# Kernel optimization log

Hardware: AMD Instinct MI355X
Metric: run time of the kernel (lower is better)

Reference implementation:

```python
import jax, jax.numpy as jnp
import numpy as np

B, T, HE, L, HD = 512, 512, 512, 64, 512

def setup_inputs() -> dict:
    key = jax.random.key(0)
    ks = jax.random.split(key, 16)
    def w(k, shape):
        return jax.random.normal(k, shape, dtype=jnp.float32) * 0.05
    z32 = lambda n: jnp.zeros((n,), jnp.float32)
    return {
        "input_tensor": jax.random.normal(ks[0], (B, T, 1), dtype=jnp.float32),
        # encoder LSTMCell (keras gate order i, f, g, o)
        "enc_W": w(ks[1], (1, 4 * HE)),
        "enc_U": w(ks[2], (HE, 4 * HE)),
        "enc_b": z32(4 * HE),
        # encoder mu / std heads
        "emu_W": w(ks[3], (HE, L)), "emu_b": z32(L),
        "estd_W": w(ks[4], (HE, L)), "estd_b": z32(L),
        # decoder first-state dense (tanh)
        "dfs_W": w(ks[5], (L, HD)), "dfs_b": z32(HD),
        # decoder LSTMCell
        "dec_W": w(ks[6], (L, 4 * HD)),
        "dec_U": w(ks[7], (HD, 4 * HD)),
        "dec_b": z32(4 * HD),
        # decoder mu / std heads (Dense(1))
        "dmu_W": w(ks[8], (HD, 1)), "dmu_b": z32(1),
        "dstd_W": w(ks[9], (HD, 1)), "dstd_b": z32(1),
    }

def _lstm_update(gates, c):
    i, f, g, o = jnp.split(gates, 4, axis=-1)
    c_new = jax.nn.sigmoid(f) * c + jax.nn.sigmoid(i) * jnp.tanh(g)
    h_new = jax.nn.sigmoid(o) * jnp.tanh(c_new)
    return h_new, c_new

def reference(input_tensor, enc_W, enc_U, enc_b, emu_W, emu_b, estd_W, estd_b,
              dfs_W, dfs_b, dec_W, dec_U, dec_b, dmu_W, dmu_b, dstd_W, dstd_b):
    x = input_tensor
    Bn, Tn = x.shape[0], x.shape[1]
    He = enc_U.shape[0]

    # ---- encoder: LSTM over time, keep final h ----
    def enc_step(carry, xt):
        h, c = carry
        gates = xt @ enc_W + h @ enc_U + enc_b
        return _lstm_update(gates, c), None
    h0 = jnp.zeros((Bn, He), x.dtype)
    (hT, _), _ = jax.lax.scan(enc_step, (h0, h0), jnp.swapaxes(x, 0, 1))

    mu_enc = hT @ emu_W + emu_b                       # [B, L]
    sigma_enc = jax.nn.softplus(hT @ estd_W + estd_b)  # [B, L]
    z = mu_enc  # call() uses reparam=False -> latent returns mu

    # ---- decoder: LSTM fed constant z each step ----
    hd = jnp.tanh(z @ dfs_W + dfs_b)                  # [B, HD]
    cd = jnp.zeros_like(hd)
    zin = z @ dec_W + dec_b                           # input projection constant over t
    def dec_step(carry, _):
        h, c = carry
        h_new, c_new = _lstm_update(zin + h @ dec_U, c)
        mu = h_new @ dmu_W + dmu_b                    # [B, 1]
        sg = h_new @ dstd_W + dstd_b
        return (h_new, c_new), (mu, sg)
    _, (mus, sgs) = jax.lax.scan(dec_step, (hd, cd), None, length=Tn)

    mu_dec = jnp.swapaxes(mus, 0, 1)                  # [B, T, 1]
    sigma_dec = jax.nn.softplus(jnp.swapaxes(sgs, 0, 1))
    return (mu_dec, sigma_dec, mu_enc, sigma_enc)
```

## Files before the change

### kernel.cpp

```cpp
#include <hip/hip_runtime.h>


#define B_   512
#define T_   512
#define H_   512
#define NGR  32
#define WPG  8
#define RPG  16
#define UPW  64

typedef _Float16 f16;
typedef _Float16 f16x8 __attribute__((ext_vector_type(8)));
typedef _Float16 f16x4 __attribute__((ext_vector_type(4)));
typedef float f32x16 __attribute__((ext_vector_type(16)));
typedef unsigned long long u64;

#define OFF_SG_DEC 262144
#define OFF_MU_ENC 524288
#define OFF_SG_ENC 557056

__device__ __forceinline__ float sigm_(float x) { return 1.f / (1.f + __expf(-x)); }
__device__ __forceinline__ float tanh_(float x) {
  float t = fabsf(x);
  float e = __expf(2.f * t);
  float r = 1.f - 2.f / (e + 1.f);
  return x < 0.f ? -r : r;
}
__device__ __forceinline__ float softplus_(float x) {
  return fmaxf(x, 0.f) + log1pf(__expf(-fabsf(x)));
}

__global__ void pack_U(const float* __restrict__ U, f16* __restrict__ Upk) {
  const int e = blockIdx.x * 256 + threadIdx.x;
  const int j = e & 7, lane = (e >> 3) & 63, ks = (e >> 9) & 31;
  const int w = (e >> 14) & 7, wg = (e >> 17) & 7;
  const int ccol = lane & 31, khalf = lane >> 5;
  const int uu = ccol >> 2, gate = ccol & 3;
  const int k = ks * 16 + khalf * 8 + j;
  const int gcol = gate * 512 + wg * UPW + w * 8 + uu;
  Upk[e] = (f16)U[k * 2048 + gcol];
}

template <int IS_DEC>
__global__ void __launch_bounds__(512, 1)
lstm_rec(const f16* __restrict__ Upk,
         const float* __restrict__ xin,
         const float* __restrict__ wa,
         const float* __restrict__ wb,
         f16* __restrict__ hbuf,
         float* __restrict__ accmu,
         float* __restrict__ accsg,
         int* __restrict__ flags) {
  const int bid = blockIdx.x;
  const int wg = (bid >> 3) & 7;
  const int g = (bid & 7) * 4 + (bid >> 6);
  const int tid = threadIdx.x;
  const int wave = tid >> 6, lane = tid & 63;
  const int R0 = g * RPG;
  const int U0 = wg * UPW;

  const int ccol = lane & 31, khalf = lane >> 5;
  f16x8 Breg[32];
#pragma unroll
  for (int ks = 0; ks < 32; ++ks) {
    const f16* p = Upk + (((wg * 8 + wave) * 32 + ks) << 9) + lane * 8;
    asm volatile("global_load_dwordx4 %0, %1, off\n\ts_waitcnt vmcnt(0)"
                 : "=v"(Breg[ks]) : "v"(p));
  }

  const int row = tid >> 4;
  const int q = (tid & 15) * 4;
  float addv[16], xw[16], dmur[4], dstdr[4];
  if (tid < 256) {
#pragma unroll
    for (int m = 0; m < 4; ++m) {
#pragma unroll
      for (int gt = 0; gt < 4; ++gt) {
        const int col = gt * 512 + U0 + q + m;
        if (IS_DEC) {
          addv[m * 4 + gt] = xin[(R0 + row) * 2048 + col];
          xw[m * 4 + gt] = 0.f;
        } else {
          addv[m * 4 + gt] = wb[col];
          xw[m * 4 + gt] = wa[col];
        }
      }
      if (IS_DEC) {
        dmur[m] = wa[U0 + q + m];
        dstdr[m] = wb[U0 + q + m];
      } else {
        dmur[m] = 0.f;
        dstdr[m] = 0.f;
      }
    }
  }

  float cst[4] = {0.f, 0.f, 0.f, 0.f};

  __shared__ __align__(16) f16 hstage[RPG * 536];
  __shared__ float gatesLds[RPG * 260];
  __shared__ float pmuLds[RPG * 17];
  __shared__ float psgLds[RPG * 17];
  __shared__ float xl[RPG * 516];

  if (!IS_DEC) {
#pragma unroll
    for (int i = 0; i < 16; ++i) {
      const int idx = tid + i * 512;
      const int r = idx >> 9, c2 = idx & 511;
      xl[r * 516 + c2] = xin[(R0 + r) * T_ + c2];
    }
    __syncthreads();
  }

  const int hrow = lane & 15;
  int* const myflag = &flags[(g * WPG + wg) * 32];
  int* const grpflags = &flags[(g * WPG) * 32];

  for (int t = 0; t < T_; ++t) {
    const u64* hsrc64 = (const u64*)(hbuf + (t & 1) * (B_ * H_) + R0 * H_);
#pragma unroll
    for (int i = 0; i < 4; ++i) {
      const int w = tid + i * 512;
      const int r = w >> 7, c8 = w & 127;
      u64 v = __hip_atomic_load(hsrc64 + w, __ATOMIC_RELAXED,
                                __HIP_MEMORY_SCOPE_AGENT);
      *(u64*)&hstage[r * 536 + c8 * 4] = v;
    }
    __syncthreads();

    f32x16 acc;
#pragma unroll
    for (int j = 0; j < 16; ++j) acc[j] = 0.f;
#pragma unroll
    for (int ks = 0; ks < 32; ++ks) {
      f16x8 a = *(const f16x8*)&hstage[hrow * 536 + ks * 16 + khalf * 8];
      acc = __builtin_amdgcn_mfma_f32_32x32x16_f16(a, Breg[ks], acc, 0, 0, 0);
    }
#pragma unroll
    for (int r = 0; r < 8; ++r) {
      const int orow = (r & 3) + 8 * (r >> 2) + 4 * khalf;
      gatesLds[orow * 260 + wave * 32 + ccol] = acc[r];
    }
    __syncthreads();

    union { f16x4 h4; u64 u; } cv;
    if (tid < 256) {
      float xv = 0.f;
      if (!IS_DEC) xv = xl[row * 516 + t];
      float hn[4];
#pragma unroll
      for (int m = 0; m < 4; ++m) {
        float ga[4];
#pragma unroll
        for (int gt = 0; gt < 4; ++gt) {
          float v = gatesLds[row * 260 + (q + m) * 4 + gt] + addv[m * 4 + gt];
          if (!IS_DEC) v += xv * xw[m * 4 + gt];
          ga[gt] = v;
        }
        const float iv = sigm_(ga[0]);
        const float fv = sigm_(ga[1]);
        const float gv = tanh_(ga[2]);
        const float ov = sigm_(ga[3]);
        const float cn = fv * cst[m] + iv * gv;
        cst[m] = cn;
        hn[m] = ov * tanh_(cn);
      }
#pragma unroll
      for (int m = 0; m < 4; ++m) cv.h4[m] = (f16)hn[m];
      f16* hdst = hbuf + ((t + 1) & 1) * (B_ * H_) + (R0 + row) * H_ + U0 + q;
      __hip_atomic_store((u64*)hdst, cv.u, __ATOMIC_RELAXED,
                         __HIP_MEMORY_SCOPE_AGENT);
      if (IS_DEC) {
        float pmu = 0.f, psg = 0.f;
#pragma unroll
        for (int m = 0; m < 4; ++m) {
          pmu += (float)cv.h4[m] * dmur[m];
          psg += (float)cv.h4[m] * dstdr[m];
        }
        pmuLds[row * 17 + (tid & 15)] = pmu;
        psgLds[row * 17 + (tid & 15)] = psg;
      }
    }

    asm volatile("s_waitcnt vmcnt(0)" ::: "memory");
    __syncthreads();
    if (t + 1 < T_ && tid == 0)
      __hip_atomic_store(myflag, t + 1, __ATOMIC_RELAXED,
                         __HIP_MEMORY_SCOPE_AGENT);

    if (IS_DEC) {
      if (tid < RPG) {
        float s = 0.f;
#pragma unroll
        for (int j = 0; j < 16; ++j) s += pmuLds[tid * 17 + j];
        unsafeAtomicAdd(&accmu[(R0 + tid) * T_ + t], s);
      } else if (tid < 2 * RPG) {
        const int rr = tid - RPG;
        float s = 0.f;
#pragma unroll
        for (int j = 0; j < 16; ++j) s += psgLds[rr * 17 + j];
        unsafeAtomicAdd(&accsg[(R0 + rr) * T_ + t], s);
      }
    }

    if (t + 1 < T_) {
      if (tid < WPG) {
        while (__hip_atomic_load(&grpflags[tid * 32], __ATOMIC_RELAXED,
                                 __HIP_MEMORY_SCOPE_AGENT) < t + 1) {
          asm volatile("s_sleep 1");
        }
      }
      __syncthreads();
    }
  }
}

__global__ void enc_heads(const f16* __restrict__ h0, const float* __restrict__ emuW,
                          const float* __restrict__ emub, const float* __restrict__ estdW,
                          const float* __restrict__ estdb, float* __restrict__ out,
                          float* __restrict__ z) {
  const int b = blockIdx.x, tid = threadIdx.x;
  __shared__ float hrow[512];
  for (int k = tid; k < 512; k += 128)
    hrow[k] = (float)h0[b * H_ + k];
  __syncthreads();
  const int head = tid >> 6, l = tid & 63;
  const float* W = head ? estdW : emuW;
  float a = 0.f;
#pragma unroll 8
  for (int k = 0; k < 512; ++k) a += hrow[k] * W[k * 64 + l];
  if (head == 0) {
    const float v = a + emub[l];
    out[OFF_MU_ENC + b * 64 + l] = v;
    z[b * 64 + l] = v;
  } else {
    out[OFF_SG_ENC + b * 64 + l] = softplus_(a + estdb[l]);
  }
}

__global__ void dec_prep(const float* __restrict__ z, const float* __restrict__ dfsW,
                         const float* __restrict__ dfsb, const float* __restrict__ decW,
                         const float* __restrict__ decb, f16* __restrict__ hbuf,
                         float* __restrict__ zin) {
  const int b = blockIdx.x, tid = threadIdx.x;
  __shared__ float zl[64];
  if (tid < 64) zl[tid] = z[b * 64 + tid];
  __syncthreads();
  for (int c = tid; c < 512; c += 256) {
    float a = dfsb[c];
#pragma unroll
    for (int l = 0; l < 64; ++l) a += zl[l] * dfsW[l * 512 + c];
    hbuf[b * H_ + c] = (f16)tanh_(a);
  }
  for (int c = tid; c < 2048; c += 256) {
    float a = decb[c];
#pragma unroll
    for (int l = 0; l < 64; ++l) a += zl[l] * decW[l * 2048 + c];
    zin[b * 2048 + c] = a;
  }
}

__global__ void finalize_k(const float* __restrict__ accmu, const float* __restrict__ accsg,
                           const float* __restrict__ dmub, const float* __restrict__ dstdb,
                           float* __restrict__ out) {
  const int i = blockIdx.x * 256 + threadIdx.x;
  out[i] = accmu[i] + dmub[0];
  out[OFF_SG_DEC + i] = softplus_(accsg[i] + dstdb[0]);
}

extern "C" void kernel_launch(void* const* d_in, const int* in_sizes, int n_in,
                              void* d_out, int out_size, void* d_ws, size_t ws_size,
                              hipStream_t stream) {
  (void)in_sizes; (void)n_in; (void)out_size; (void)ws_size;
  const float* x     = (const float*)d_in[0];
  const float* encW  = (const float*)d_in[1];
  const float* encU  = (const float*)d_in[2];
  const float* encb  = (const float*)d_in[3];
  const float* emuW  = (const float*)d_in[4];
  const float* emub  = (const float*)d_in[5];
  const float* estdW = (const float*)d_in[6];
  const float* estdb = (const float*)d_in[7];
  const float* dfsW  = (const float*)d_in[8];
  const float* dfsb  = (const float*)d_in[9];
  const float* decW  = (const float*)d_in[10];
  const float* decb  = (const float*)d_in[12];
  const float* decU  = (const float*)d_in[11];
  const float* dmuW  = (const float*)d_in[13];
  const float* dmub  = (const float*)d_in[14];
  const float* dstdW = (const float*)d_in[15];
  const float* dstdb = (const float*)d_in[16];

  char* ws = (char*)d_ws;
  f16* hbuf    = (f16*)(ws + 0);
  float* accmu = (float*)(ws + (1u << 20));
  float* accsg = (float*)(ws + (2u << 20));
  int* flags   = (int*)(ws + (3u << 20));
  f16* UpkE    = (f16*)(ws + (3u << 20) + 65536);
  float* zin   = (float*)(ws + (3u << 20) + 65536);
  f16* UpkD    = (f16*)(ws + (7u << 20) + 65536);
  float* z     = (float*)(ws + (9u << 20) + 65536);
  float* out   = (float*)d_out;

  hipMemsetAsync(d_ws, 0, (3u << 20) + 65536, stream);

  hipLaunchKernelGGL(pack_U, dim3(4096), dim3(256), 0, stream, encU, UpkE);
  hipLaunchKernelGGL(pack_U, dim3(4096), dim3(256), 0, stream, decU, UpkD);

  hipLaunchKernelGGL((lstm_rec<0>), dim3(256), dim3(512), 0, stream,
                     UpkE, x, encW, encb, hbuf, (float*)nullptr, (float*)nullptr,
                     flags);
  hipLaunchKernelGGL(enc_heads, dim3(512), dim3(128), 0, stream,
                     hbuf, emuW, emub, estdW, estdb, out, z);
  hipLaunchKernelGGL(dec_prep, dim3(512), dim3(256), 0, stream,
                     z, dfsW, dfsb, decW, decb, hbuf, zin);
  hipLaunchKernelGGL((lstm_rec<1>), dim3(256), dim3(512), 0, stream,
                     UpkD, zin, dmuW, dstdW, hbuf, accmu, accsg, flags + 8192);
  hipLaunchKernelGGL(finalize_k, dim3(1024), dim3(256), 0, stream,
                     accmu, accsg, dmub, dstdb, out);
}
```

Before: 4.233 ms.

## Replace per-step flag barrier with generation-tagged h values polled directly

Each fp16 hidden value is now stored in a 32-bit word with a 16-bit generation tag, so consumers spin on the h data itself until every word carries the current step's tag. This removes the separate flag store, the vmcnt drain, and the flag-polling barrier. The next step's loads are issued early, hstage is double-buffered, and the decoder output heads are computed one step late from staged h with wave shuffles instead of atomics, plus a tail kernel for the last step. The cost is twice the bytes per h exchange and busy polling without sleeps.

```diff
diff --git a/kernel.cpp b/kernel.cpp
--- a/kernel.cpp
+++ b/kernel.cpp
@@ -11,9 +11,9 @@
 
 typedef _Float16 f16;
 typedef _Float16 f16x8 __attribute__((ext_vector_type(8)));
-typedef _Float16 f16x4 __attribute__((ext_vector_type(4)));
 typedef float f32x16 __attribute__((ext_vector_type(16)));
 typedef unsigned long long u64;
+typedef unsigned int u32;
 
 #define OFF_SG_DEC 262144
 #define OFF_MU_ENC 524288
@@ -28,6 +28,12 @@
 }
 __device__ __forceinline__ float softplus_(float x) {
   return fmaxf(x, 0.f) + log1pf(__expf(-fabsf(x)));
+}
+__device__ __forceinline__ int fresh_(u64 w, u32 g) {
+  return ((u32)(w >> 48) == g) & (((u32)(w >> 16) & 0xffffu) == g);
+}
+__device__ __forceinline__ u32 packh_(u64 w) {
+  return (u32)(w & 0xffffu) | (((u32)(w >> 32) & 0xffffu) << 16);
 }
 
 __global__ void pack_U(const float* __restrict__ U, f16* __restrict__ Upk) {
@@ -47,10 +53,9 @@
          const float* __restrict__ xin,
          const float* __restrict__ wa,
          const float* __restrict__ wb,
-         f16* __restrict__ hbuf,
+         u32* __restrict__ hbuf,
          float* __restrict__ accmu,
-         float* __restrict__ accsg,
-         int* __restrict__ flags) {
+         float* __restrict__ accsg) {
   const int bid = blockIdx.x;
   const int wg = (bid >> 3) & 7;
   const int g = (bid & 7) * 4 + (bid >> 6);
@@ -58,6 +63,7 @@
   const int wave = tid >> 6, lane = tid & 63;
   const int R0 = g * RPG;
   const int U0 = wg * UPW;
+  const u32 GB = IS_DEC ? 0x8000u : 0u;
 
   const int ccol = lane & 31, khalf = lane >> 5;
   f16x8 Breg[32];
@@ -70,7 +76,7 @@
 
   const int row = tid >> 4;
   const int q = (tid & 15) * 4;
-  float addv[16], xw[16], dmur[4], dstdr[4];
+  float addv[16], xw[16];
   if (tid < 256) {
 #pragma unroll
     for (int m = 0; m < 4; ++m) {
@@ -85,22 +91,21 @@
           xw[m * 4 + gt] = wa[col];
         }
       }
-      if (IS_DEC) {
-        dmur[m] = wa[U0 + q + m];
-        dstdr[m] = wb[U0 + q + m];
-      } else {
-        dmur[m] = 0.f;
-        dstdr[m] = 0.f;
-      }
+    }
+  }
+  float wmu[8], wsg[8];
+  if (IS_DEC) {
+#pragma unroll
+    for (int j = 0; j < 8; ++j) {
+      wmu[j] = wa[lane * 8 + j];
+      wsg[j] = wb[lane * 8 + j];
     }
   }
 
   float cst[4] = {0.f, 0.f, 0.f, 0.f};
 
-  __shared__ __align__(16) f16 hstage[RPG * 536];
+  __shared__ __align__(16) f16 hstage[2][RPG * 536];
   __shared__ float gatesLds[RPG * 260];
-  __shared__ float pmuLds[RPG * 17];
-  __shared__ float psgLds[RPG * 17];
   __shared__ float xl[RPG * 516];
 
   if (!IS_DEC) {
@@ -113,20 +118,43 @@
     __syncthreads();
   }
 
+  int srow[8], scol[8], gidx[8];
+#pragma unroll
+  for (int i = 0; i < 8; ++i) {
+    const int w = tid + i * 512;
+    srow[i] = w >> 8; scol[i] = w & 255;
+    gidx[i] = (R0 + srow[i]) * 256 + scol[i];
+  }
+  const u64* hb64 = (const u64*)hbuf;
   const int hrow = lane & 15;
-  int* const myflag = &flags[(g * WPG + wg) * 32];
-  int* const grpflags = &flags[(g * WPG) * 32];
+
+  u64 wr[8];
+#pragma unroll
+  for (int i = 0; i < 8; ++i)
+    wr[i] = __hip_atomic_load(hb64 + gidx[i], __ATOMIC_RELAXED,
+                              __HIP_MEMORY_SCOPE_AGENT);
+  asm volatile("" ::: "memory");
 
   for (int t = 0; t < T_; ++t) {
-    const u64* hsrc64 = (const u64*)(hbuf + (t & 1) * (B_ * H_) + R0 * H_);
-#pragma unroll
-    for (int i = 0; i < 4; ++i) {
-      const int w = tid + i * 512;
-      const int r = w >> 7, c8 = w & 127;
-      u64 v = __hip_atomic_load(hsrc64 + w, __ATOMIC_RELAXED,
-                                __HIP_MEMORY_SCOPE_AGENT);
-      *(u64*)&hstage[r * 536 + c8 * 4] = v;
-    }
+    const int b0 = (t & 1) * 131072;
+    const int b1 = ((t + 1) & 1) * 131072;
+    const int c1 = ((t + 1) & 1) * 262144;
+    const u32 gr = GB + (u32)t, gn = gr + 1u;
+
+    for (;;) {
+      int f = 1;
+#pragma unroll
+      for (int i = 0; i < 8; ++i) f &= fresh_(wr[i], gr);
+      if (f) break;
+#pragma unroll
+      for (int i = 0; i < 8; ++i)
+        wr[i] = __hip_atomic_load(hb64 + b0 + gidx[i], __ATOMIC_RELAXED,
+                                  __HIP_MEMORY_SCOPE_AGENT);
+    }
+    f16* const sb = hstage[t & 1];
+#pragma unroll
+    for (int i = 0; i < 8; ++i)
+      *(u32*)&sb[srow[i] * 536 + scol[i] * 2] = packh_(wr[i]);
     __syncthreads();
 
     f32x16 acc;
@@ -134,7 +162,7 @@
     for (int j = 0; j < 16; ++j) acc[j] = 0.f;
 #pragma unroll
     for (int ks = 0; ks < 32; ++ks) {
-      f16x8 a = *(const f16x8*)&hstage[hrow * 536 + ks * 16 + khalf * 8];
+      f16x8 a = *(const f16x8*)&sb[hrow * 536 + ks * 16 + khalf * 8];
       acc = __builtin_amdgcn_mfma_f32_32x32x16_f16(a, Breg[ks], acc, 0, 0, 0);
     }
 #pragma unroll
@@ -144,7 +172,6 @@
     }
     __syncthreads();
 
-    union { f16x4 h4; u64 u; } cv;
     if (tid < 256) {
       float xv = 0.f;
       if (!IS_DEC) xv = xl[row * 516 + t];
@@ -166,64 +193,78 @@
         cst[m] = cn;
         hn[m] = ov * tanh_(cn);
       }
-#pragma unroll
-      for (int m = 0; m < 4; ++m) cv.h4[m] = (f16)hn[m];
-      f16* hdst = hbuf + ((t + 1) & 1) * (B_ * H_) + (R0 + row) * H_ + U0 + q;
-      __hip_atomic_store((u64*)hdst, cv.u, __ATOMIC_RELAXED,
-                         __HIP_MEMORY_SCOPE_AGENT);
-      if (IS_DEC) {
-        float pmu = 0.f, psg = 0.f;
-#pragma unroll
-        for (int m = 0; m < 4; ++m) {
-          pmu += (float)cv.h4[m] * dmur[m];
-          psg += (float)cv.h4[m] * dstdr[m];
-        }
-        pmuLds[row * 17 + (tid & 15)] = pmu;
-        psgLds[row * 17 + (tid & 15)] = psg;
-      }
-    }
-
-    asm volatile("s_waitcnt vmcnt(0)" ::: "memory");
-    __syncthreads();
-    if (t + 1 < T_ && tid == 0)
-      __hip_atomic_store(myflag, t + 1, __ATOMIC_RELAXED,
-                         __HIP_MEMORY_SCOPE_AGENT);
-
-    if (IS_DEC) {
-      if (tid < RPG) {
-        float s = 0.f;
-#pragma unroll
-        for (int j = 0; j < 16; ++j) s += pmuLds[tid * 17 + j];
-        unsafeAtomicAdd(&accmu[(R0 + tid) * T_ + t], s);
-      } else if (tid < 2 * RPG) {
-        const int rr = tid - RPG;
-        float s = 0.f;
-#pragma unroll
-        for (int j = 0; j < 16; ++j) s += psgLds[rr * 17 + j];
-        unsafeAtomicAdd(&accsg[(R0 + rr) * T_ + t], s);
-      }
-    }
-
-    if (t + 1 < T_) {
-      if (tid < WPG) {
-        while (__hip_atomic_load(&grpflags[tid * 32], __ATOMIC_RELAXED,
-                                 __HIP_MEMORY_SCOPE_AGENT) < t + 1) {
-          asm volatile("s_sleep 1");
-        }
-      }
-      __syncthreads();
-    }
-  }
-}
-
-__global__ void enc_heads(const f16* __restrict__ h0, const float* __restrict__ emuW,
+      union { f16 h; unsigned short u; } hc0, hc1, hc2, hc3;
+      hc0.h = (f16)hn[0]; hc1.h = (f16)hn[1];
+      hc2.h = (f16)hn[2]; hc3.h = (f16)hn[3];
+      const u64 tg = (u64)gn << 16;
+      const u64 w0 = (tg | hc0.u) | (((tg | hc1.u)) << 32);
+      const u64 w1 = (tg | hc2.u) | (((tg | hc3.u)) << 32);
+      u64* hdst = (u64*)(hbuf + c1 + (R0 + row) * 512 + U0 + q);
+      __hip_atomic_store(hdst, w0, __ATOMIC_RELAXED, __HIP_MEMORY_SCOPE_AGENT);
+      __hip_atomic_store(hdst + 1, w1, __ATOMIC_RELAXED, __HIP_MEMORY_SCOPE_AGENT);
+    }
+
+#pragma unroll
+    for (int i = 0; i < 8; ++i)
+      wr[i] = __hip_atomic_load(hb64 + b1 + gidx[i], __ATOMIC_RELAXED,
+                                __HIP_MEMORY_SCOPE_AGENT);
+    asm volatile("" ::: "memory");
+
+    if (IS_DEC && t >= 1 && wave < 2) {
+      const int hr = 2 * wg + wave;
+      const f16x8 hv = *(const f16x8*)&sb[hr * 536 + lane * 8];
+      float smu = 0.f, ssg = 0.f;
+#pragma unroll
+      for (int j = 0; j < 8; ++j) {
+        const float hq = (float)hv[j];
+        smu += hq * wmu[j]; ssg += hq * wsg[j];
+      }
+#pragma unroll
+      for (int o = 32; o; o >>= 1) {
+        smu += __shfl_xor(smu, o); ssg += __shfl_xor(ssg, o);
+      }
+      if (lane == 0) {
+        accmu[(R0 + hr) * 512 + (t - 1)] = smu;
+        accsg[(R0 + hr) * 512 + (t - 1)] = ssg;
+      }
+    }
+  }
+}
+
+__global__ void dec_tail(const u32* __restrict__ hbuf, const float* __restrict__ dmuW,
+                         const float* __restrict__ dstdW, float* __restrict__ accmu,
+                         float* __restrict__ accsg) {
+  const int r = blockIdx.x, lane = threadIdx.x;
+  float smu = 0.f, ssg = 0.f;
+#pragma unroll
+  for (int j = 0; j < 8; ++j) {
+    union { unsigned short u; f16 h; } c;
+    c.u = (unsigned short)(hbuf[r * 512 + lane * 8 + j] & 0xffffu);
+    const float hq = (float)c.h;
+    smu += hq * dmuW[lane * 8 + j];
+    ssg += hq * dstdW[lane * 8 + j];
+  }
+#pragma unroll
+  for (int o = 32; o; o >>= 1) {
+    smu += __shfl_xor(smu, o); ssg += __shfl_xor(ssg, o);
+  }
+  if (lane == 0) {
+    accmu[r * 512 + 511] = smu;
+    accsg[r * 512 + 511] = ssg;
+  }
+}
+
+__global__ void enc_heads(const u32* __restrict__ h0, const float* __restrict__ emuW,
                           const float* __restrict__ emub, const float* __restrict__ estdW,
                           const float* __restrict__ estdb, float* __restrict__ out,
                           float* __restrict__ z) {
   const int b = blockIdx.x, tid = threadIdx.x;
   __shared__ float hrow[512];
-  for (int k = tid; k < 512; k += 128)
-    hrow[k] = (float)h0[b * H_ + k];
+  for (int k = tid; k < 512; k += 128) {
+    union { unsigned short u; f16 h; } c;
+    c.u = (unsigned short)(h0[b * 512 + k] & 0xffffu);
+    hrow[k] = (float)c.h;
+  }
   __syncthreads();
   const int head = tid >> 6, l = tid & 63;
   const float* W = head ? estdW : emuW;
@@ -241,7 +282,7 @@
 
 __global__ void dec_prep(const float* __restrict__ z, const float* __restrict__ dfsW,
                          const float* __restrict__ dfsb, const float* __restrict__ decW,
-                         const float* __restrict__ decb, f16* __restrict__ hbuf,
+                         const float* __restrict__ decb, u32* __restrict__ hbuf,
                          float* __restrict__ zin) {
   const int b = blockIdx.x, tid = threadIdx.x;
   __shared__ float zl[64];
@@ -251,7 +292,8 @@
     float a = dfsb[c];
 #pragma unroll
     for (int l = 0; l < 64; ++l) a += zl[l] * dfsW[l * 512 + c];
-    hbuf[b * H_ + c] = (f16)tanh_(a);
+    union { f16 h; unsigned short u; } hc; hc.h = (f16)tanh_(a);
+    hbuf[b * 512 + c] = (0x8000u << 16) | (u32)hc.u;
   }
   for (int c = tid; c < 2048; c += 256) {
     float a = decb[c];
@@ -284,38 +326,38 @@
   const float* dfsW  = (const float*)d_in[8];
   const float* dfsb  = (const float*)d_in[9];
   const float* decW  = (const float*)d_in[10];
+  const float* decU  = (const float*)d_in[11];
   const float* decb  = (const float*)d_in[12];
-  const float* decU  = (const float*)d_in[11];
   const float* dmuW  = (const float*)d_in[13];
   const float* dmub  = (const float*)d_in[14];
   const float* dstdW = (const float*)d_in[15];
   const float* dstdb = (const float*)d_in[16];
 
   char* ws = (char*)d_ws;
-  f16* hbuf    = (f16*)(ws + 0);
-  float* accmu = (float*)(ws + (1u << 20));
-  float* accsg = (float*)(ws + (2u << 20));
-  int* flags   = (int*)(ws + (3u << 20));
-  f16* UpkE    = (f16*)(ws + (3u << 20) + 65536);
-  float* zin   = (float*)(ws + (3u << 20) + 65536);
-  f16* UpkD    = (f16*)(ws + (7u << 20) + 65536);
-  float* z     = (float*)(ws + (9u << 20) + 65536);
+  u32*   hbuf  = (u32*)(ws + 0);
+  float* accmu = (float*)(ws + (2u << 20));
+  float* accsg = (float*)(ws + (3u << 20));
+  f16*   UpkE  = (f16*)(ws + (4u << 20));
+  float* zin   = (float*)(ws + (4u << 20));
+  f16*   UpkD  = (f16*)(ws + (8u << 20));
+  float* z     = (float*)(ws + (10u << 20));
   float* out   = (float*)d_out;
 
-  hipMemsetAsync(d_ws, 0, (3u << 20) + 65536, stream);
+  hipMemsetAsync(d_ws, 0, 2u << 20, stream);
 
   hipLaunchKernelGGL(pack_U, dim3(4096), dim3(256), 0, stream, encU, UpkE);
   hipLaunchKernelGGL(pack_U, dim3(4096), dim3(256), 0, stream, decU, UpkD);
 
   hipLaunchKernelGGL((lstm_rec<0>), dim3(256), dim3(512), 0, stream,
-                     UpkE, x, encW, encb, hbuf, (float*)nullptr, (float*)nullptr,
-                     flags);
+                     UpkE, x, encW, encb, hbuf, (float*)nullptr, (float*)nullptr);
   hipLaunchKernelGGL(enc_heads, dim3(512), dim3(128), 0, stream,
                      hbuf, emuW, emub, estdW, estdb, out, z);
   hipLaunchKernelGGL(dec_prep, dim3(512), dim3(256), 0, stream,
                      z, dfsW, dfsb, decW, decb, hbuf, zin);
   hipLaunchKernelGGL((lstm_rec<1>), dim3(256), dim3(512), 0, stream,
-                     UpkD, zin, dmuW, dstdW, hbuf, accmu, accsg, flags + 8192);
+                     UpkD, zin, dmuW, dstdW, hbuf, accmu, accsg);
+  hipLaunchKernelGGL(dec_tail, dim3(512), dim3(64), 0, stream,
+                     hbuf, dmuW, dstdW, accmu, accsg);
   hipLaunchKernelGGL(finalize_k, dim3(1024), dim3(256), 0, stream,
                      accmu, accsg, dmub, dstdb, out);
 }
```

Result: slower. 4.896 ms (+15.7%).

## Replace encoder flag barrier with generation-tagged h values and two-half pipelining

Applied to the files above, without the earlier changes.

The encoder recurrence becomes its own kernel. Each h value is stored as a 32-bit word carrying the fp16 value plus a step tag, so consumers poll the data words directly for freshness instead of waiting on per-group flags and a separate barrier. Each block splits its 16 rows into two 8-row halves and interleaves them, so loading one half's h overlaps the MFMA and gate work of the other. This removes the flag store/poll round trip and adds overlap, at the cost of doubling the h buffer size, spin-polling on data words, and running MFMAs on half-empty tiles.

```diff
diff --git a/kernel.cpp b/kernel.cpp
--- a/kernel.cpp
+++ b/kernel.cpp
@@ -14,6 +14,7 @@
 typedef _Float16 f16x4 __attribute__((ext_vector_type(4)));
 typedef float f32x16 __attribute__((ext_vector_type(16)));
 typedef unsigned long long u64;
+typedef unsigned int u32;
 
 #define OFF_SG_DEC 262144
 #define OFF_MU_ENC 524288
@@ -28,6 +29,12 @@
 }
 __device__ __forceinline__ float softplus_(float x) {
   return fmaxf(x, 0.f) + log1pf(__expf(-fabsf(x)));
+}
+__device__ __forceinline__ int fresh_(u64 w, u32 g) {
+  return ((u32)(w >> 48) == g) & (((u32)(w >> 16) & 0xffffu) == g);
+}
+__device__ __forceinline__ u32 packh_(u64 w) {
+  return (u32)(w & 0xffffu) | (((u32)(w >> 32) & 0xffffu) << 16);
 }
 
 __global__ void pack_U(const float* __restrict__ U, f16* __restrict__ Upk) {
@@ -41,12 +48,172 @@
   Upk[e] = (f16)U[k * 2048 + gcol];
 }
 
-template <int IS_DEC>
 __global__ void __launch_bounds__(512, 1)
-lstm_rec(const f16* __restrict__ Upk,
+lstm_enc(const f16* __restrict__ Upk,
          const float* __restrict__ xin,
          const float* __restrict__ wa,
          const float* __restrict__ wb,
+         u32* __restrict__ hbuf) {
+  const int bid = blockIdx.x;
+  const int s = bid >> 3;
+  const int j = (bid & 7) * 4 + (s & 3);
+  const int wg = s >> 2;
+  const int tid = threadIdx.x, wave = tid >> 6, lane = tid & 63;
+  const int U0 = wg * 64;
+  const int RA = j * 16, RB = j * 16 + 8;
+  const int ccol = lane & 31, khalf = lane >> 5;
+
+  f16x8 Breg[32];
+#pragma unroll
+  for (int ks = 0; ks < 32; ++ks) {
+    const f16* p = Upk + (((wg * 8 + wave) * 32 + ks) << 9) + lane * 8;
+    asm volatile("global_load_dwordx4 %0, %1, off\n\ts_waitcnt vmcnt(0)"
+                 : "=v"(Breg[ks]) : "v"(p));
+  }
+
+  const int erow = tid >> 6, eu = tid & 63;
+  float xwv[4], bias[4];
+#pragma unroll
+  for (int gt = 0; gt < 4; ++gt) {
+    const int col = gt * 512 + U0 + eu;
+    bias[gt] = wb[col];
+    xwv[gt] = wa[col];
+  }
+
+  float cA = 0.f, cB = 0.f;
+
+  __shared__ __align__(16) f16 bufA[8 * 520];
+  __shared__ __align__(16) f16 bufB[8 * 520];
+  __shared__ __align__(16) float gatesL[8 * 264];
+
+  int lrow[4], lcol[4], gidxA[4], gidxB[4];
+#pragma unroll
+  for (int i = 0; i < 4; ++i) {
+    const int w = tid + i * 512;
+    lrow[i] = w >> 8; lcol[i] = w & 255;
+    gidxA[i] = (RA + lrow[i]) * 256 + lcol[i];
+    gidxB[i] = (RB + lrow[i]) * 256 + lcol[i];
+  }
+  const u64* hb64 = (const u64*)hbuf;
+
+  u64 wAr[4], wBr[4];
+#pragma unroll
+  for (int i = 0; i < 4; ++i)
+    wAr[i] = __hip_atomic_load(hb64 + gidxA[i], __ATOMIC_RELAXED,
+                               __HIP_MEMORY_SCOPE_AGENT);
+  asm volatile("" ::: "memory");
+
+  for (int t = 0; t < T_; ++t) {
+    const int b0 = (t & 1) * 131072;
+    const int b1 = ((t + 1) & 1) * 131072;
+    const int c1 = ((t + 1) & 1) * 262144;
+    const u32 gr = (u32)t, gn = (u32)t + 1u;
+
+    while (!(fresh_(wAr[0], gr) & fresh_(wAr[1], gr) &
+             fresh_(wAr[2], gr) & fresh_(wAr[3], gr))) {
+#pragma unroll
+      for (int i = 0; i < 4; ++i)
+        wAr[i] = __hip_atomic_load(hb64 + b0 + gidxA[i], __ATOMIC_RELAXED,
+                                   __HIP_MEMORY_SCOPE_AGENT);
+    }
+#pragma unroll
+    for (int i = 0; i < 4; ++i)
+      *(u32*)&bufA[lrow[i] * 520 + lcol[i] * 2] = packh_(wAr[i]);
+    __syncthreads();
+
+#pragma unroll
+    for (int i = 0; i < 4; ++i)
+      wBr[i] = __hip_atomic_load(hb64 + b0 + gidxB[i], __ATOMIC_RELAXED,
+                                 __HIP_MEMORY_SCOPE_AGENT);
+    asm volatile("" ::: "memory");
+
+    {
+      f32x16 acc;
+#pragma unroll
+      for (int q = 0; q < 16; ++q) acc[q] = 0.f;
+#pragma unroll
+      for (int ks = 0; ks < 32; ++ks) {
+        f16x8 a = *(const f16x8*)&bufA[(lane & 7) * 520 + ks * 16 + khalf * 8];
+        acc = __builtin_amdgcn_mfma_f32_32x32x16_f16(a, Breg[ks], acc, 0, 0, 0);
+      }
+#pragma unroll
+      for (int r = 0; r < 4; ++r)
+        gatesL[(r + 4 * khalf) * 264 + wave * 32 + ccol] = acc[r];
+    }
+    __syncthreads();
+
+    {
+      const float4 g4 = *(const float4*)&gatesL[erow * 264 + (eu >> 3) * 32 + (eu & 7) * 4];
+      const float xv = xin[(RA + erow) * T_ + t];
+      const float ga0 = g4.x + bias[0] + xv * xwv[0];
+      const float ga1 = g4.y + bias[1] + xv * xwv[1];
+      const float ga2 = g4.z + bias[2] + xv * xwv[2];
+      const float ga3 = g4.w + bias[3] + xv * xwv[3];
+      const float cn = sigm_(ga1) * cA + sigm_(ga0) * tanh_(ga2);
+      cA = cn;
+      const float hn = sigm_(ga3) * tanh_(cn);
+      union { f16 h; unsigned short u; } hc; hc.h = (f16)hn;
+      __hip_atomic_store(hbuf + c1 + (RA + erow) * 512 + U0 + eu,
+                         (gn << 16) | (u32)hc.u, __ATOMIC_RELAXED,
+                         __HIP_MEMORY_SCOPE_AGENT);
+    }
+
+    while (!(fresh_(wBr[0], gr) & fresh_(wBr[1], gr) &
+             fresh_(wBr[2], gr) & fresh_(wBr[3], gr))) {
+#pragma unroll
+      for (int i = 0; i < 4; ++i)
+        wBr[i] = __hip_atomic_load(hb64 + b0 + gidxB[i], __ATOMIC_RELAXED,
+                                   __HIP_MEMORY_SCOPE_AGENT);
+    }
+#pragma unroll
+    for (int i = 0; i < 4; ++i)
+      *(u32*)&bufB[lrow[i] * 520 + lcol[i] * 2] = packh_(wBr[i]);
+    __syncthreads();
+
+#pragma unroll
+    for (int i = 0; i < 4; ++i)
+      wAr[i] = __hip_atomic_load(hb64 + b1 + gidxA[i], __ATOMIC_RELAXED,
+                                 __HIP_MEMORY_SCOPE_AGENT);
+    asm volatile("" ::: "memory");
+
+    {
+      f32x16 acc;
+#pragma unroll
+      for (int q = 0; q < 16; ++q) acc[q] = 0.f;
+#pragma unroll
+      for (int ks = 0; ks < 32; ++ks) {
+        f16x8 a = *(const f16x8*)&bufB[(lane & 7) * 520 + ks * 16 + khalf * 8];
+        acc = __builtin_amdgcn_mfma_f32_32x32x16_f16(a, Breg[ks], acc, 0, 0, 0);
+      }
+#pragma unroll
+      for (int r = 0; r < 4; ++r)
+        gatesL[(r + 4 * khalf) * 264 + wave * 32 + ccol] = acc[r];
+    }
+    __syncthreads();
+
+    {
+      const float4 g4 = *(const float4*)&gatesL[erow * 264 + (eu >> 3) * 32 + (eu & 7) * 4];
+      const float xv = xin[(RB + erow) * T_ + t];
+      const float ga0 = g4.x + bias[0] + xv * xwv[0];
+      const float ga1 = g4.y + bias[1] + xv * xwv[1];
+      const float ga2 = g4.z + bias[2] + xv * xwv[2];
+      const float ga3 = g4.w + bias[3] + xv * xwv[3];
+      const float cn = sigm_(ga1) * cB + sigm_(ga0) * tanh_(ga2);
+      cB = cn;
+      const float hn = sigm_(ga3) * tanh_(cn);
+      union { f16 h; unsigned short u; } hc; hc.h = (f16)hn;
+      __hip_atomic_store(hbuf + c1 + (RB + erow) * 512 + U0 + eu,
+                         (gn << 16) | (u32)hc.u, __ATOMIC_RELAXED,
+                         __HIP_MEMORY_SCOPE_AGENT);
+    }
+  }
+}
+
+__global__ void __launch_bounds__(512, 1)
+lstm_dec(const f16* __restrict__ Upk,
+         const float* __restrict__ zin,
+         const float* __restrict__ wmu_,
+         const float* __restrict__ wsg_,
          f16* __restrict__ hbuf,
          float* __restrict__ accmu,
          float* __restrict__ accsg,
@@ -70,28 +237,15 @@
 
   const int row = tid >> 4;
   const int q = (tid & 15) * 4;
-  float addv[16], xw[16], dmur[4], dstdr[4];
+  float addv[16], dmur[4], dstdr[4];
   if (tid < 256) {
 #pragma unroll
     for (int m = 0; m < 4; ++m) {
 #pragma unroll
-      for (int gt = 0; gt < 4; ++gt) {
-        const int col = gt * 512 + U0 + q + m;
-        if (IS_DEC) {
-          addv[m * 4 + gt] = xin[(R0 + row) * 2048 + col];
-          xw[m * 4 + gt] = 0.f;
-        } else {
-          addv[m * 4 + gt] = wb[col];
-          xw[m * 4 + gt] = wa[col];
-        }
-      }
-      if (IS_DEC) {
-        dmur[m] = wa[U0 + q + m];
-        dstdr[m] = wb[U0 + q + m];
-      } else {
-        dmur[m] = 0.f;
-        dstdr[m] = 0.f;
-      }
+      for (int gt = 0; gt < 4; ++gt)
+        addv[m * 4 + gt] = zin[(R0 + row) * 2048 + gt * 512 + U0 + q + m];
+      dmur[m] = wmu_[U0 + q + m];
+      dstdr[m] = wsg_[U0 + q + m];
     }
   }
 
@@ -101,17 +255,6 @@
   __shared__ float gatesLds[RPG * 260];
   __shared__ float pmuLds[RPG * 17];
   __shared__ float psgLds[RPG * 17];
-  __shared__ float xl[RPG * 516];
-
-  if (!IS_DEC) {
-#pragma unroll
-    for (int i = 0; i < 16; ++i) {
-      const int idx = tid + i * 512;
-      const int r = idx >> 9, c2 = idx & 511;
-      xl[r * 516 + c2] = xin[(R0 + r) * T_ + c2];
-    }
-    __syncthreads();
-  }
 
   const int hrow = lane & 15;
   int* const myflag = &flags[(g * WPG + wg) * 32];
@@ -146,18 +289,13 @@
 
     union { f16x4 h4; u64 u; } cv;
     if (tid < 256) {
-      float xv = 0.f;
-      if (!IS_DEC) xv = xl[row * 516 + t];
       float hn[4];
 #pragma unroll
       for (int m = 0; m < 4; ++m) {
         float ga[4];
 #pragma unroll
-        for (int gt = 0; gt < 4; ++gt) {
-          float v = gatesLds[row * 260 + (q + m) * 4 + gt] + addv[m * 4 + gt];
-          if (!IS_DEC) v += xv * xw[m * 4 + gt];
-          ga[gt] = v;
-        }
+        for (int gt = 0; gt < 4; ++gt)
+          ga[gt] = gatesLds[row * 260 + (q + m) * 4 + gt] + addv[m * 4 + gt];
         const float iv = sigm_(ga[0]);
         const float fv = sigm_(ga[1]);
         const float gv = tanh_(ga[2]);
@@ -171,16 +309,14 @@
       f16* hdst = hbuf + ((t + 1) & 1) * (B_ * H_) + (R0 + row) * H_ + U0 + q;
       __hip_atomic_store((u64*)hdst, cv.u, __ATOMIC_RELAXED,
                          __HIP_MEMORY_SCOPE_AGENT);
-      if (IS_DEC) {
-        float pmu = 0.f, psg = 0.f;
-#pragma unroll
-        for (int m = 0; m < 4; ++m) {
-          pmu += (float)cv.h4[m] * dmur[m];
-          psg += (float)cv.h4[m] * dstdr[m];
-        }
-        pmuLds[row * 17 + (tid & 15)] = pmu;
-        psgLds[row * 17 + (tid & 15)] = psg;
+      float pmu = 0.f, psg = 0.f;
+#pragma unroll
+      for (int m = 0; m < 4; ++m) {
+        pmu += (float)cv.h4[m] * dmur[m];
+        psg += (float)cv.h4[m] * dstdr[m];
       }
+      pmuLds[row * 17 + (tid & 15)] = pmu;
+      psgLds[row * 17 + (tid & 15)] = psg;
     }
 
     asm volatile("s_waitcnt vmcnt(0)" ::: "memory");
@@ -189,19 +325,17 @@
       __hip_atomic_store(myflag, t + 1, __ATOMIC_RELAXED,
                          __HIP_MEMORY_SCOPE_AGENT);
 
-    if (IS_DEC) {
-      if (tid < RPG) {
-        float s = 0.f;
-#pragma unroll
-        for (int j = 0; j < 16; ++j) s += pmuLds[tid * 17 + j];
-        unsafeAtomicAdd(&accmu[(R0 + tid) * T_ + t], s);
-      } else if (tid < 2 * RPG) {
-        const int rr = tid - RPG;
-        float s = 0.f;
-#pragma unroll
-        for (int j = 0; j < 16; ++j) s += psgLds[rr * 17 + j];
-        unsafeAtomicAdd(&accsg[(R0 + rr) * T_ + t], s);
-      }
+    if (tid < RPG) {
+      float s = 0.f;
+#pragma unroll
+      for (int j = 0; j < 16; ++j) s += pmuLds[tid * 17 + j];
+      unsafeAtomicAdd(&accmu[(R0 + tid) * T_ + t], s);
+    } else if (tid < 2 * RPG) {
+      const int rr = tid - RPG;
+      float s = 0.f;
+#pragma unroll
+      for (int j = 0; j < 16; ++j) s += psgLds[rr * 17 + j];
+      unsafeAtomicAdd(&accsg[(R0 + rr) * T_ + t], s);
     }
 
     if (t + 1 < T_) {
@@ -216,14 +350,17 @@
   }
 }
 
-__global__ void enc_heads(const f16* __restrict__ h0, const float* __restrict__ emuW,
+__global__ void enc_heads(const u32* __restrict__ h0, const float* __restrict__ emuW,
                           const float* __restrict__ emub, const float* __restrict__ estdW,
                           const float* __restrict__ estdb, float* __restrict__ out,
                           float* __restrict__ z) {
   const int b = blockIdx.x, tid = threadIdx.x;
   __shared__ float hrow[512];
-  for (int k = tid; k < 512; k += 128)
-    hrow[k] = (float)h0[b * H_ + k];
+  for (int k = tid; k < 512; k += 128) {
+    union { unsigned short u; f16 h; } c;
+    c.u = (unsigned short)(h0[b * 512 + k] & 0xffffu);
+    hrow[k] = (float)c.h;
+  }
   __syncthreads();
   const int head = tid >> 6, l = tid & 63;
   const float* W = head ? estdW : emuW;
@@ -284,38 +421,38 @@
   const float* dfsW  = (const float*)d_in[8];
   const float* dfsb  = (const float*)d_in[9];
   const float* decW  = (const float*)d_in[10];
+  const float* decU  = (const float*)d_in[11];
   const float* decb  = (const float*)d_in[12];
-  const float* decU  = (const float*)d_in[11];
   const float* dmuW  = (const float*)d_in[13];
   const float* dmub  = (const float*)d_in[14];
   const float* dstdW = (const float*)d_in[15];
   const float* dstdb = (const float*)d_in[16];
 
   char* ws = (char*)d_ws;
-  f16* hbuf    = (f16*)(ws + 0);
-  float* accmu = (float*)(ws + (1u << 20));
-  float* accsg = (float*)(ws + (2u << 20));
-  int* flags   = (int*)(ws + (3u << 20));
-  f16* UpkE    = (f16*)(ws + (3u << 20) + 65536);
-  float* zin   = (float*)(ws + (3u << 20) + 65536);
-  f16* UpkD    = (f16*)(ws + (7u << 20) + 65536);
-  float* z     = (float*)(ws + (9u << 20) + 65536);
+  u32*   hbufG = (u32*)(ws + 0);
+  float* accmu = (float*)(ws + (2u << 20));
+  float* accsg = (float*)(ws + (3u << 20));
+  int*   flags = (int*)(ws + (4u << 20));
+  f16*   hbufF = (f16*)(ws + (4u << 20) + 65536);
+  f16*   UpkE  = (f16*)(ws + (5u << 20) + 65536);
+  float* zin   = (float*)(ws + (5u << 20) + 65536);
+  f16*   UpkD  = (f16*)(ws + (9u << 20) + 65536);
+  float* z     = (float*)(ws + (11u << 20) + 65536);
   float* out   = (float*)d_out;
 
-  hipMemsetAsync(d_ws, 0, (3u << 20) + 65536, stream);
+  hipMemsetAsync(d_ws, 0, (4u << 20) + 65536, stream);
 
   hipLaunchKernelGGL(pack_U, dim3(4096), dim3(256), 0, stream, encU, UpkE);
   hipLaunchKernelGGL(pack_U, dim3(4096), dim3(256), 0, stream, decU, UpkD);
 
-  hipLaunchKernelGGL((lstm_rec<0>), dim3(256), dim3(512), 0, stream,
-                     UpkE, x, encW, encb, hbuf, (float*)nullptr, (float*)nullptr,
-                     flags);
+  hipLaunchKernelGGL(lstm_enc, dim3(256), dim3(512), 0, stream,
+                     UpkE, x, encW, encb, hbufG);
   hipLaunchKernelGGL(enc_heads, dim3(512), dim3(128), 0, stream,
-                     hbuf, emuW, emub, estdW, estdb, out, z);
+                     hbufG, emuW, emub, estdW, estdb, out, z);
   hipLaunchKernelGGL(dec_prep, dim3(512), dim3(256), 0, stream,
-                     z, dfsW, dfsb, decW, decb, hbuf, zin);
-  hipLaunchKernelGGL((lstm_rec<1>), dim3(256), dim3(512), 0, stream,
-                     UpkD, zin, dmuW, dstdW, hbuf, accmu, accsg, flags + 8192);
+                     z, dfsW, dfsb, decW, decb, hbufF, zin);
+  hipLaunchKernelGGL(lstm_dec, dim3(256), dim3(512), 0, stream,
+                     UpkD, zin, dmuW, dstdW, hbufF, accmu, accsg, flags);
   hipLaunchKernelGGL(finalize_k, dim3(1024), dim3(256), 0, stream,
                      accmu, accsg, dmub, dstdb, out);
 }
```

Result: slower. 4.509 ms (+6.5%).

## Move step barrier to per-wave flag polling and reduce decoder heads via shuffles

Applied to the files above, without the earlier changes.

Drops the block-wide flag wait and trailing __syncthreads at the end of each timestep. Each wave now polls the group flags itself with a wave-wide vote before it loads h, so the barrier that follows the staging load does the ordering. The decoder mu/std partial dot products are now reduced with xor shuffles inside 16-lane groups instead of through LDS arrays plus a separate __syncthreads, and the atomics are issued directly. The aim is fewer block barriers and LDS round trips on the serial critical path, at the cost of every wave spinning on global flags.

```diff
diff --git a/kernel.cpp b/kernel.cpp
--- a/kernel.cpp
+++ b/kernel.cpp
@@ -99,8 +99,6 @@
 
   __shared__ __align__(16) f16 hstage[RPG * 536];
   __shared__ float gatesLds[RPG * 260];
-  __shared__ float pmuLds[RPG * 17];
-  __shared__ float psgLds[RPG * 17];
   __shared__ float xl[RPG * 516];
 
   if (!IS_DEC) {
@@ -118,6 +116,17 @@
   int* const grpflags = &flags[(g * WPG) * 32];
 
   for (int t = 0; t < T_; ++t) {
+    if (t) {
+      for (;;) {
+        int fv = t;
+        if (lane < WPG)
+          fv = __hip_atomic_load(&grpflags[lane * 32], __ATOMIC_RELAXED,
+                                 __HIP_MEMORY_SCOPE_AGENT);
+        if (__all(fv >= t)) break;
+        asm volatile("s_sleep 1");
+      }
+    }
+
     const u64* hsrc64 = (const u64*)(hbuf + (t & 1) * (B_ * H_) + R0 * H_);
 #pragma unroll
     for (int i = 0; i < 4; ++i) {
@@ -144,11 +153,10 @@
     }
     __syncthreads();
 
-    union { f16x4 h4; u64 u; } cv;
+    float hn[4];
     if (tid < 256) {
       float xv = 0.f;
       if (!IS_DEC) xv = xl[row * 516 + t];
-      float hn[4];
 #pragma unroll
       for (int m = 0; m < 4; ++m) {
         float ga[4];
@@ -166,21 +174,12 @@
         cst[m] = cn;
         hn[m] = ov * tanh_(cn);
       }
+      union { f16x4 h4; u64 u; } cv;
 #pragma unroll
       for (int m = 0; m < 4; ++m) cv.h4[m] = (f16)hn[m];
       f16* hdst = hbuf + ((t + 1) & 1) * (B_ * H_) + (R0 + row) * H_ + U0 + q;
       __hip_atomic_store((u64*)hdst, cv.u, __ATOMIC_RELAXED,
                          __HIP_MEMORY_SCOPE_AGENT);
-      if (IS_DEC) {
-        float pmu = 0.f, psg = 0.f;
-#pragma unroll
-        for (int m = 0; m < 4; ++m) {
-          pmu += (float)cv.h4[m] * dmur[m];
-          psg += (float)cv.h4[m] * dstdr[m];
-        }
-        pmuLds[row * 17 + (tid & 15)] = pmu;
-        psgLds[row * 17 + (tid & 15)] = psg;
-      }
     }
 
     asm volatile("s_waitcnt vmcnt(0)" ::: "memory");
@@ -189,29 +188,22 @@
       __hip_atomic_store(myflag, t + 1, __ATOMIC_RELAXED,
                          __HIP_MEMORY_SCOPE_AGENT);
 
-    if (IS_DEC) {
-      if (tid < RPG) {
-        float s = 0.f;
-#pragma unroll
-        for (int j = 0; j < 16; ++j) s += pmuLds[tid * 17 + j];
-        unsafeAtomicAdd(&accmu[(R0 + tid) * T_ + t], s);
-      } else if (tid < 2 * RPG) {
-        const int rr = tid - RPG;
-        float s = 0.f;
-#pragma unroll
-        for (int j = 0; j < 16; ++j) s += psgLds[rr * 17 + j];
-        unsafeAtomicAdd(&accsg[(R0 + rr) * T_ + t], s);
-      }
-    }
-
-    if (t + 1 < T_) {
-      if (tid < WPG) {
-        while (__hip_atomic_load(&grpflags[tid * 32], __ATOMIC_RELAXED,
-                                 __HIP_MEMORY_SCOPE_AGENT) < t + 1) {
-          asm volatile("s_sleep 1");
-        }
-      }
-      __syncthreads();
+    if (IS_DEC && tid < 256) {
+      float pmu = 0.f, psg = 0.f;
+#pragma unroll
+      for (int m = 0; m < 4; ++m) {
+        pmu += (float)((f16)hn[m]) * dmur[m];
+        psg += (float)((f16)hn[m]) * dstdr[m];
+      }
+#pragma unroll
+      for (int o = 1; o < 16; o <<= 1) {
+        pmu += __shfl_xor(pmu, o);
+        psg += __shfl_xor(psg, o);
+      }
+      if ((tid & 15) == 0) {
+        unsafeAtomicAdd(&accmu[(R0 + row) * T_ + t], pmu);
+        unsafeAtomicAdd(&accsg[(R0 + row) * T_ + t], psg);
+      }
     }
   }
 }
@@ -284,8 +276,8 @@
   const float* dfsW  = (const float*)d_in[8];
   const float* dfsb  = (const float*)d_in[9];
   const float* decW  = (const float*)d_in[10];
+  const float* decU  = (const float*)d_in[11];
   const float* decb  = (const float*)d_in[12];
-  const float* decU  = (const float*)d_in[11];
   const float* dmuW  = (const float*)d_in[13];
   const float* dmub  = (const float*)d_in[14];
   const float* dstdW = (const float*)d_in[15];
```

Result: slower. 4.403 ms (+4.0%).
